# Kernel tuning notes

Hardware: AMD Instinct MI355X
Metric: run time of the kernel (lower is better)

The kernel has to match this reference:

```python
import jax, jax.numpy as jnp
import numpy as np

DM = 1024      # dmodel
HQK = 1024     # heads*dq == heads*dk == heads*dv
FF = 4096
VOCAB = 32000
NCAT = 75
DK = 64        # per-head dk used for 1/sqrt(dk) scaling
UNK_IDX = 1
EPS = 1e-5


def pos_encoding(n, dm):
    pos = jnp.arange(n, dtype=jnp.float32)[:, None]                  # [n,1]
    power = jnp.arange(0, dm, 2, dtype=jnp.float32) / dm             # [dm/2]
    denom = jnp.power(10000.0, power)                                # [dm/2]
    ang = pos / denom                                                # [n,dm/2]
    # even cols = sin, odd cols = cos (interleaved)
    return jnp.stack([jnp.sin(ang), jnp.cos(ang)], axis=-1).reshape(n, dm)


def layernorm(x, g, b):
    mu = jnp.mean(x, axis=-1, keepdims=True)
    var = jnp.var(x, axis=-1, keepdims=True)
    return (x - mu) * jax.lax.rsqrt(var + EPS) * g + b


def setup_inputs() -> dict:
    key = jax.random.key(0)
    ks = jax.random.split(key, 16)
    s = 0.02
    inp = {
        "input_indices": jax.random.randint(ks[0], (8, 2048), 0, VOCAB),
        "emb": jax.random.normal(ks[1], (VOCAB, DM), jnp.float32) * s,
        "Wq": jax.random.normal(ks[2], (DM, HQK), jnp.float32) * s,
        "bq": jnp.zeros((HQK,), jnp.float32),
        "Wk": jax.random.normal(ks[3], (DM, HQK), jnp.float32) * s,
        "bk": jnp.zeros((HQK,), jnp.float32),
        "Wv": jax.random.normal(ks[4], (DM, HQK), jnp.float32) * s,
        "bv": jnp.zeros((HQK,), jnp.float32),
        "Wu": jax.random.normal(ks[5], (HQK, DM), jnp.float32) * s,
        "bu": jnp.zeros((DM,), jnp.float32),
        "g1": jnp.ones((DM,), jnp.float32),
        "be1": jnp.zeros((DM,), jnp.float32),
        "W1": jax.random.normal(ks[6], (DM, FF), jnp.float32) * s,
        "b1": jnp.zeros((FF,), jnp.float32),
        "W2": jax.random.normal(ks[7], (FF, DM), jnp.float32) * s,
        "b2": jnp.zeros((DM,), jnp.float32),
        "g2": jnp.ones((DM,), jnp.float32),
        "be2": jnp.zeros((DM,), jnp.float32),
        "W3": jax.random.normal(ks[8], (DM, DM // 2), jnp.float32) * s,
        "b3": jnp.zeros((DM // 2,), jnp.float32),
        "W4": jax.random.normal(ks[9], (DM // 2, NCAT), jnp.float32) * s,
        "b4": jnp.zeros((NCAT,), jnp.float32),
        "g3": jnp.ones((NCAT,), jnp.float32),
        "be3": jnp.zeros((NCAT,), jnp.float32),
    }
    return inp


def reference(input_indices, emb, Wq, bq, Wk, bk, Wv, bv, Wu, bu, g1, be1,
              W1, b1, W2, b2, g2, be2, W3, b3, W4, b4, g3, be3):
    d, n = input_indices.shape
    idx = jnp.where(input_indices >= VOCAB, UNK_IDX, input_indices)
    x = emb[idx] + pos_encoding(n, DM)[None]                          # [d,n,dm]
    # attention WITHOUT softmax: scores = QK^T/sqrt(dk); attn = scores @ V
    q = x @ Wq + bq
    k = x @ Wk + bk
    v = x @ Wv + bv
    scores = jnp.einsum('bnd,bmd->bnm', q, k) / (DK ** 0.5)           # [d,n,n]
    attn = jnp.einsum('bnm,bmd->bnd', scores, v)                      # [d,n,hdv]
    u = attn @ Wu + bu
    h1 = layernorm(x + u, g1, be1)
    ffo = jax.nn.relu(h1 @ W1 + b1) @ W2 + b2
    h2 = layernorm(h1 + ffo, g2, be2)
    logits = jax.nn.relu(h2 @ W3 + b3) @ W4 + b4                      # [d,n,75]
    return jax.nn.sigmoid(layernorm(logits, g3, be3))
```

## Files before the change

kernel.cpp:

```cpp
#include <hip/hip_runtime.h>
#include <hip/hip_fp16.h>
#include <math.h>

#define DM    1024
#define FFD   4096
#define VOCAB 32000
#define NCAT  75
#define UNK_IDX 1
#define EPS   1e-5f
#define NB    8
#define SEQ   2048
#define T_TOK (NB*SEQ)

using u16   = unsigned short;
using half_t = _Float16;
using half8 = __attribute__((ext_vector_type(8))) _Float16;
using f32x4 = __attribute__((ext_vector_type(4))) float;

struct alignas(8) h4 { half_t s[4]; };

__device__ __forceinline__ void async16(const half_t* g, half_t* l) {
    __builtin_amdgcn_global_load_lds(
        (const __attribute__((address_space(1))) void*)g,
        (__attribute__((address_space(3))) void*)l,
        16, 0, 0);
}

__global__ __launch_bounds__(256)
void embed_pos_kernel(const int* __restrict__ idx,
                      const float* __restrict__ emb,
                      float* __restrict__ xf, half_t* __restrict__ xh)
{
    int gid = blockIdx.x * blockDim.x + threadIdx.x;
    if (gid >= T_TOK * DM) return;
    int dcol = gid & (DM - 1);
    int tok  = gid >> 10;
    int t    = tok & (SEQ - 1);
    int id = idx[tok];
    if (id >= VOCAB || id < 0) id = UNK_IDX;
    int p = dcol >> 1;
    float power = (float)p / 512.0f;
    float denom = powf(10000.0f, power);
    float ang = (float)t / denom;
    float pe = (dcol & 1) ? cosf(ang) : sinf(ang);
    float v = emb[(long long)id * DM + dcol] + pe;
    xf[gid] = v;
    xh[gid] = (half_t)v;
}

__global__ __launch_bounds__(256)
void transpose_h_kernel(const float* __restrict__ in, half_t* __restrict__ out,
                        int K, int N, int Npad)
{
    __shared__ float t[32][33];
    int n0 = blockIdx.x * 32, k0 = blockIdx.y * 32;
    int tx = threadIdx.x & 31, ty = threadIdx.x >> 5;
#pragma unroll
    for (int i = 0; i < 4; i++) {
        int k = k0 + ty + i * 8, n = n0 + tx;
        t[ty + i * 8][tx] = (k < K && n < N) ? in[(long long)k * N + n] : 0.f;
    }
    __syncthreads();
#pragma unroll
    for (int i = 0; i < 4; i++) {
        int n = n0 + ty + i * 8, k = k0 + tx;
        if (n < Npad && k < K)
            out[(long long)n * K + k] = (half_t)t[tx][ty + i * 8];
    }
}

__global__ __launch_bounds__(128)
void pad_bias_kernel(const float* __restrict__ b, float* __restrict__ bp)
{
    int i = threadIdx.x;
    bp[i] = (i < NCAT) ? b[i] : 0.f;
}

template<int OUT_MODE>
__global__ __launch_bounds__(256)
void gemm_nt(const half_t* __restrict__ A, const half_t* __restrict__ B,
             const float* __restrict__ bias, void* __restrict__ Cout,
             int M, int N, int K, int ld,
             long long sA, long long sB, long long sC,
             float scale, int do_relu)
{
    A += (long long)blockIdx.z * sA;
    B += (long long)blockIdx.z * sB;
    const int tid  = threadIdx.x;
    const int lane = tid & 63;
    const int w    = tid >> 6;
    const int wm   = w >> 1, wn = w & 1;
    const long long row0 = (long long)blockIdx.y * 128;
    const long long col0 = (long long)blockIdx.x * 128;

    __shared__ half_t smem[4 * 4096];
    half_t* const As = smem;
    half_t* const Bs = smem + 2 * 4096;

    f32x4 acc[4][4];
    const f32x4 zero = {0.f, 0.f, 0.f, 0.f};
#pragma unroll
    for (int i = 0; i < 4; i++)
#pragma unroll
        for (int j = 0; j < 4; j++) acc[i][j] = zero;

    const int ldrow = lane >> 2;
    const int swcol = (((lane & 3) << 3)) ^ ((ldrow & 3) << 3);
    const int fr    = lane & 15;
    const int kk8   = (lane >> 4) << 3;

    const int KT = K / 32;

#define ISSUE(k0, buf)                                                         \
    {                                                                          \
        _Pragma("unroll")                                                      \
        for (int it = 0; it < 2; ++it) {                                       \
            int rb = (it * 4 + w) * 16;                                        \
            long long ao = (row0 + rb + ldrow) * (long long)ld + (k0) + swcol; \
            long long bo = (col0 + rb + ldrow) * (long long)ld + (k0) + swcol; \
            async16(A + ao, As + (buf) * 4096 + rb * 32);                      \
            async16(B + bo, Bs + (buf) * 4096 + rb * 32);                      \
        }                                                                      \
    }

    ISSUE(0, 0);
    for (int kt = 0; kt < KT; ++kt) {
        const int cur = kt & 1;
        __syncthreads();
        if (kt + 1 < KT) ISSUE((kt + 1) * 32, cur ^ 1);

        half8 af[4], bf[4];
#pragma unroll
        for (int i = 0; i < 4; ++i) {
            int r   = wm * 64 + i * 16 + fr;
            int off = cur * 4096 + r * 32 + (kk8 ^ ((r & 3) << 3));
            af[i] = *(const half8*)(As + off);
        }
#pragma unroll
        for (int j = 0; j < 4; ++j) {
            int r   = wn * 64 + j * 16 + fr;
            int off = cur * 4096 + r * 32 + (kk8 ^ ((r & 3) << 3));
            bf[j] = *(const half8*)(Bs + off);
        }
#pragma unroll
        for (int i = 0; i < 4; ++i)
#pragma unroll
            for (int j = 0; j < 4; ++j)
                acc[i][j] = __builtin_amdgcn_mfma_f32_16x16x32_f16(
                    af[i], bf[j], acc[i][j], 0, 0, 0);
    }
#undef ISSUE

    const int qr = (lane >> 4) * 4;
    const int lc = lane & 15;
#pragma unroll
    for (int i = 0; i < 4; ++i) {
#pragma unroll
        for (int j = 0; j < 4; ++j) {
            long long gc = col0 + wn * 64 + j * 16 + lc;
            float bv = bias ? bias[gc] : 0.f;
            if (OUT_MODE == 2) {
                long long gr = row0 + wm * 64 + i * 16 + qr;
                int b  = (int)(gr >> 11);
                int tl = (int)(gr & (SEQ - 1));
                h4 pk;
#pragma unroll
                for (int r = 0; r < 4; ++r) {
                    float f = acc[i][j][r] * scale + bv;
                    if (do_relu) f = fmaxf(f, 0.f);
                    pk.s[r] = (half_t)f;
                }
                half_t* C = (half_t*)Cout;
                *(h4*)(C + (long long)b * N * SEQ + gc * SEQ + tl) = pk;
            } else if (OUT_MODE == 1) {
                half_t* C = (half_t*)Cout + blockIdx.z * sC;
#pragma unroll
                for (int r = 0; r < 4; ++r) {
                    long long gr = row0 + wm * 64 + i * 16 + qr + r;
                    float f = acc[i][j][r] * scale + bv;
                    if (do_relu) f = fmaxf(f, 0.f);
                    C[gr * N + gc] = (half_t)f;
                }
            } else {
                float* C = (float*)Cout + blockIdx.z * sC;
#pragma unroll
                for (int r = 0; r < 4; ++r) {
                    long long gr = row0 + wm * 64 + i * 16 + qr + r;
                    float f = acc[i][j][r] * scale + bv;
                    if (do_relu) f = fmaxf(f, 0.f);
                    C[gr * N + gc] = f;
                }
            }
        }
    }
}

__global__ __launch_bounds__(256)
void reduce2_bias_kernel(const float* __restrict__ s0, const float* __restrict__ s1,
                         const float* __restrict__ bias, float* __restrict__ out,
                         int n4)
{
    int i = blockIdx.x * blockDim.x + threadIdx.x;
    if (i >= n4) return;
    float4 a = ((const float4*)s0)[i];
    float4 b = ((const float4*)s1)[i];
    int c4 = (i * 4) & (DM - 1);
    float4 bb = *(const float4*)(bias + c4);
    float4 r;
    r.x = a.x + b.x + bb.x;
    r.y = a.y + b.y + bb.y;
    r.z = a.z + b.z + bb.z;
    r.w = a.w + b.w + bb.w;
    ((float4*)out)[i] = r;
}

__global__ __launch_bounds__(256)
void add_ln_kernel(const float* __restrict__ X, const float* __restrict__ Y,
                   const float* __restrict__ g, const float* __restrict__ b,
                   float* __restrict__ outf, half_t* __restrict__ outh)
{
    int row = blockIdx.x;
    int tid = threadIdx.x;
    const float* xr = X + (long long)row * DM;
    const float* yr = Y + (long long)row * DM;
    float v[4];
    float s = 0.f, s2 = 0.f;
#pragma unroll
    for (int i = 0; i < 4; i++) {
        int c = tid + i * 256;
        v[i] = xr[c] + yr[c];
        s  += v[i];
        s2 += v[i] * v[i];
    }
#pragma unroll
    for (int o = 1; o < 64; o <<= 1) {
        s  += __shfl_xor(s,  o, 64);
        s2 += __shfl_xor(s2, o, 64);
    }
    __shared__ float rs[4], rs2[4], stats[2];
    int wid = tid >> 6;
    if ((tid & 63) == 0) { rs[wid] = s; rs2[wid] = s2; }
    __syncthreads();
    if (tid == 0) {
        float S  = rs[0] + rs[1] + rs[2] + rs[3];
        float S2 = rs2[0] + rs2[1] + rs2[2] + rs2[3];
        float mean = S / (float)DM;
        float var  = S2 / (float)DM - mean * mean;
        stats[0] = mean;
        stats[1] = rsqrtf(var + EPS);
    }
    __syncthreads();
    float mean = stats[0], rstd = stats[1];
#pragma unroll
    for (int i = 0; i < 4; i++) {
        int c = tid + i * 256;
        float o = (v[i] - mean) * rstd * g[c] + b[c];
        if (outf) outf[(long long)row * DM + c] = o;
        outh[(long long)row * DM + c] = (half_t)o;
    }
}

__global__ __launch_bounds__(64)
void ln75_sigmoid_kernel(const float* __restrict__ L,
                         const float* __restrict__ g, const float* __restrict__ b,
                         float* __restrict__ out)
{
    int row = blockIdx.x;
    int t   = threadIdx.x;
    const float* lr = L + (long long)row * 128;
    float e0 = (t < NCAT) ? lr[t] : 0.f;
    float e1 = (t + 64 < NCAT) ? lr[t + 64] : 0.f;
    float s  = e0 + e1;
    float s2 = e0 * e0 + e1 * e1;
#pragma unroll
    for (int o = 1; o < 64; o <<= 1) {
        s  += __shfl_xor(s,  o, 64);
        s2 += __shfl_xor(s2, o, 64);
    }
    float mean = s / (float)NCAT;
    float var  = s2 / (float)NCAT - mean * mean;
    float rstd = rsqrtf(var + EPS);
    if (t < NCAT) {
        float z = (e0 - mean) * rstd * g[t] + b[t];
        out[(long long)row * NCAT + t] = 1.f / (1.f + expf(-z));
    }
    if (t + 64 < NCAT) {
        float z = (e1 - mean) * rstd * g[t + 64] + b[t + 64];
        out[(long long)row * NCAT + t + 64] = 1.f / (1.f + expf(-z));
    }
}

extern "C" void kernel_launch(void* const* d_in, const int* in_sizes, int n_in,
                              void* d_out, int out_size, void* d_ws, size_t ws_size,
                              hipStream_t stream)
{
    const int*   idx = (const int*)  d_in[0];
    const float* emb = (const float*)d_in[1];
    const float* Wq  = (const float*)d_in[2];
    const float* bq  = (const float*)d_in[3];
    const float* Wk  = (const float*)d_in[4];
    const float* bk  = (const float*)d_in[5];
    const float* Wv  = (const float*)d_in[6];
    const float* bv  = (const float*)d_in[7];
    const float* Wu  = (const float*)d_in[8];
    const float* bu  = (const float*)d_in[9];
    const float* g1  = (const float*)d_in[10];
    const float* be1 = (const float*)d_in[11];
    const float* W1  = (const float*)d_in[12];
    const float* b1  = (const float*)d_in[13];
    const float* W2  = (const float*)d_in[14];
    const float* b2  = (const float*)d_in[15];
    const float* g2  = (const float*)d_in[16];
    const float* be2 = (const float*)d_in[17];
    const float* W3  = (const float*)d_in[18];
    const float* b3  = (const float*)d_in[19];
    const float* W4  = (const float*)d_in[20];
    const float* b4  = (const float*)d_in[21];
    const float* g3  = (const float*)d_in[22];
    const float* be3 = (const float*)d_in[23];

    const long long TD  = (long long)T_TOK * DM;
    char* p = (char*)d_ws;
    char* R_A = p; p += TD * 4;
    char* R_B = p; p += TD * 2;
    char* R_C = p; p += TD * 2;
    char* R_D = p; p += TD * 4;
    char* R_E = p; p += TD * 4;
    char* R_F = p; p += (long long)NB * DM * DM * 4;
    char* R_G = p; p += (long long)T_TOK * 128 * 4;
    half_t* Wqh = (half_t*)p; p += DM*DM*2;
    half_t* Wkh = (half_t*)p; p += DM*DM*2;
    half_t* Wvh = (half_t*)p; p += DM*DM*2;
    half_t* Wuh = (half_t*)p; p += DM*DM*2;
    half_t* W1h = (half_t*)p; p += (long long)FFD*DM*2;
    half_t* W2h = (half_t*)p; p += (long long)DM*FFD*2;
    half_t* W3h = (half_t*)p; p += 512*DM*2;
    half_t* W4h = (half_t*)p; p += 128*512*2;
    float*  b4p = (float*)p;  p += 128*4;

    float*  Xf   = (float*)R_A;
    float*  ffo  = (float*)R_A;
    half_t* Xh   = (half_t*)R_B;
    half_t* attn = (half_t*)R_B;
    half_t* h2h  = (half_t*)R_B;
    half_t* Qh   = (half_t*)R_C;
    half_t* h1h  = (half_t*)R_C;
    half_t* Kt   = (half_t*)R_D;
    float*  u    = (float*)R_D;
    half_t* f1h  = (half_t*)R_D;
    half_t* Vt   = (half_t*)R_E;
    float*  h1f  = (float*)R_E;
    half_t* ktv  = (half_t*)R_F;
    float*  slc  = (float*)R_F;
    half_t* l1h  = (half_t*)R_F;
    float*  LOG  = (float*)R_G;
    float*  out  = (float*)d_out;

    dim3 blk(256);

    transpose_h_kernel<<<dim3(32, 32),  blk, 0, stream>>>(Wq, Wqh, DM, DM, DM);
    transpose_h_kernel<<<dim3(32, 32),  blk, 0, stream>>>(Wk, Wkh, DM, DM, DM);
    transpose_h_kernel<<<dim3(32, 32),  blk, 0, stream>>>(Wv, Wvh, DM, DM, DM);
    transpose_h_kernel<<<dim3(32, 32),  blk, 0, stream>>>(Wu, Wuh, DM, DM, DM);
    transpose_h_kernel<<<dim3(128, 32), blk, 0, stream>>>(W1, W1h, DM, FFD, FFD);
    transpose_h_kernel<<<dim3(32, 128), blk, 0, stream>>>(W2, W2h, FFD, DM, DM);
    transpose_h_kernel<<<dim3(16, 32),  blk, 0, stream>>>(W3, W3h, DM, 512, 512);
    transpose_h_kernel<<<dim3(4, 16),   blk, 0, stream>>>(W4, W4h, 512, NCAT, 128);
    pad_bias_kernel<<<1, 128, 0, stream>>>(b4, b4p);

    embed_pos_kernel<<<(T_TOK * DM + 255) / 256, blk, 0, stream>>>(idx, emb, Xf, Xh);

    gemm_nt<1><<<dim3(8, 128, 1), blk, 0, stream>>>(Xh, Wqh, bq, Qh,
        T_TOK, DM, DM, DM, 0, 0, 0, 1.f, 0);
    gemm_nt<2><<<dim3(8, 128, 1), blk, 0, stream>>>(Xh, Wkh, bk, Kt,
        T_TOK, DM, DM, DM, 0, 0, 0, 1.f, 0);
    gemm_nt<2><<<dim3(8, 128, 1), blk, 0, stream>>>(Xh, Wvh, bv, Vt,
        T_TOK, DM, DM, DM, 0, 0, 0, 1.f, 0);

    gemm_nt<1><<<dim3(8, 8, NB), blk, 0, stream>>>(Vt, Kt, nullptr, ktv,
        DM, DM, SEQ, SEQ, (long long)DM * SEQ, (long long)DM * SEQ, (long long)DM * DM, 0.125f, 0);

    gemm_nt<1><<<dim3(8, 16, NB), blk, 0, stream>>>(Qh, ktv, nullptr, attn,
        SEQ, DM, DM, DM, (long long)SEQ * DM, (long long)DM * DM, (long long)SEQ * DM, 1.f, 0);

    gemm_nt<0><<<dim3(8, 128, 1), blk, 0, stream>>>(attn, Wuh, bu, u,
        T_TOK, DM, DM, DM, 0, 0, 0, 1.f, 0);

    add_ln_kernel<<<T_TOK, blk, 0, stream>>>(Xf, u, g1, be1, h1f, h1h);

    for (int c = 0; c < 4; c++) {
        const half_t* h1c  = h1h + (long long)c * 4096 * DM;
        float*        ffoc = ffo + (long long)c * 4096 * DM;
        gemm_nt<1><<<dim3(32, 32, 1), blk, 0, stream>>>(h1c, W1h, b1, f1h,
            4096, FFD, DM, DM, 0, 0, 0, 1.f, 1);
        gemm_nt<0><<<dim3(8, 32, 2), blk, 0, stream>>>(f1h, W2h, nullptr, slc,
            4096, DM, 2048, FFD, 2048, 2048, (long long)4096 * DM, 1.f, 0);
        reduce2_bias_kernel<<<(4096 * DM / 4 + 255) / 256, blk, 0, stream>>>(
            slc, slc + (long long)4096 * DM, b2, ffoc, 4096 * DM / 4);
    }

    add_ln_kernel<<<T_TOK, blk, 0, stream>>>(h1f, ffo, g2, be2, nullptr, h2h);

    gemm_nt<1><<<dim3(4, 128, 1), blk, 0, stream>>>(h2h, W3h, b3, l1h,
        T_TOK, 512, DM, DM, 0, 0, 0, 1.f, 1);
    gemm_nt<0><<<dim3(1, 128, 1), blk, 0, stream>>>(l1h, W4h, b4p, LOG,
        T_TOK, 128, 512, 512, 0, 0, 0, 1.f, 0);

    ln75_sigmoid_kernel<<<T_TOK, 64, 0, stream>>>(LOG, g3, be3, out);
}
```

Baseline: 1.253 ms.

## Fold Wu into per-batch K^T V matrix, fuse residual, drop split-K FFN

Precomputes the positional encoding table once and vectorizes embedding and layernorm with float4 accesses. Reassociates the attention output projection, computing (K^T V)·Wu per batch so the per-token Wu GEMM disappears, and adds the residual inside the GEMM epilogue. The FFN now runs in two larger chunks without split-K, which removes the reduce kernel. Extra per-batch DMxDM GEMMs are added, and the fp16 rounding of the folded matrix may change numerics slightly.

Measured after the change: 1.212 ms. 1.03x faster.

```diff
diff --git a/kernel.cpp b/kernel.cpp
--- a/kernel.cpp
+++ b/kernel.cpp
@@ -27,25 +27,38 @@
 }
 
 __global__ __launch_bounds__(256)
-void embed_pos_kernel(const int* __restrict__ idx,
-                      const float* __restrict__ emb,
-                      float* __restrict__ xf, half_t* __restrict__ xh)
+void pe_kernel(float* __restrict__ pe)
 {
     int gid = blockIdx.x * blockDim.x + threadIdx.x;
-    if (gid >= T_TOK * DM) return;
+    if (gid >= SEQ * DM) return;
     int dcol = gid & (DM - 1);
-    int tok  = gid >> 10;
-    int t    = tok & (SEQ - 1);
-    int id = idx[tok];
-    if (id >= VOCAB || id < 0) id = UNK_IDX;
+    int t    = gid >> 10;
     int p = dcol >> 1;
     float power = (float)p / 512.0f;
     float denom = powf(10000.0f, power);
     float ang = (float)t / denom;
-    float pe = (dcol & 1) ? cosf(ang) : sinf(ang);
-    float v = emb[(long long)id * DM + dcol] + pe;
-    xf[gid] = v;
-    xh[gid] = (half_t)v;
+    pe[gid] = (dcol & 1) ? cosf(ang) : sinf(ang);
+}
+
+__global__ __launch_bounds__(256)
+void embed_pos_kernel(const int* __restrict__ idx,
+                      const float* __restrict__ emb,
+                      const float* __restrict__ pe,
+                      float* __restrict__ xf, half_t* __restrict__ xh)
+{
+    int gid4 = blockIdx.x * blockDim.x + threadIdx.x;
+    if (gid4 >= T_TOK * DM / 4) return;
+    int tok = gid4 >> 8;
+    int c4  = (gid4 & 255) << 2;
+    int t   = tok & (SEQ - 1);
+    int id = idx[tok];
+    if (id >= VOCAB || id < 0) id = UNK_IDX;
+    float4 e = *(const float4*)(emb + (long long)id * DM + c4);
+    float4 q = *(const float4*)(pe + (long long)t * DM + c4);
+    float4 v = make_float4(e.x + q.x, e.y + q.y, e.z + q.z, e.w + q.w);
+    *(float4*)(xf + (long long)tok * DM + c4) = v;
+    h4 pk = {{(half_t)v.x, (half_t)v.y, (half_t)v.z, (half_t)v.w}};
+    *(h4*)(xh + (long long)tok * DM + c4) = pk;
 }
 
 __global__ __launch_bounds__(256)
@@ -79,7 +92,8 @@
 template<int OUT_MODE>
 __global__ __launch_bounds__(256)
 void gemm_nt(const half_t* __restrict__ A, const half_t* __restrict__ B,
-             const float* __restrict__ bias, void* __restrict__ Cout,
+             const float* __restrict__ bias, const float* __restrict__ resid,
+             void* __restrict__ Cout,
              int M, int N, int K, int ld,
              long long sA, long long sB, long long sC,
              float scale, int do_relu)
@@ -153,6 +167,7 @@
 
     const int qr = (lane >> 4) * 4;
     const int lc = lane & 15;
+    const float* rz = resid ? resid + (long long)blockIdx.z * sC : nullptr;
 #pragma unroll
     for (int i = 0; i < 4; ++i) {
 #pragma unroll
@@ -188,6 +203,7 @@
                     long long gr = row0 + wm * 64 + i * 16 + qr + r;
                     float f = acc[i][j][r] * scale + bv;
                     if (do_relu) f = fmaxf(f, 0.f);
+                    if (rz) f += rz[gr * N + gc];
                     C[gr * N + gc] = f;
                 }
             }
@@ -196,42 +212,19 @@
 }
 
 __global__ __launch_bounds__(256)
-void reduce2_bias_kernel(const float* __restrict__ s0, const float* __restrict__ s1,
-                         const float* __restrict__ bias, float* __restrict__ out,
-                         int n4)
-{
-    int i = blockIdx.x * blockDim.x + threadIdx.x;
-    if (i >= n4) return;
-    float4 a = ((const float4*)s0)[i];
-    float4 b = ((const float4*)s1)[i];
-    int c4 = (i * 4) & (DM - 1);
-    float4 bb = *(const float4*)(bias + c4);
-    float4 r;
-    r.x = a.x + b.x + bb.x;
-    r.y = a.y + b.y + bb.y;
-    r.z = a.z + b.z + bb.z;
-    r.w = a.w + b.w + bb.w;
-    ((float4*)out)[i] = r;
-}
-
-__global__ __launch_bounds__(256)
 void add_ln_kernel(const float* __restrict__ X, const float* __restrict__ Y,
                    const float* __restrict__ g, const float* __restrict__ b,
                    float* __restrict__ outf, half_t* __restrict__ outh)
 {
     int row = blockIdx.x;
     int tid = threadIdx.x;
-    const float* xr = X + (long long)row * DM;
-    const float* yr = Y + (long long)row * DM;
-    float v[4];
-    float s = 0.f, s2 = 0.f;
-#pragma unroll
-    for (int i = 0; i < 4; i++) {
-        int c = tid + i * 256;
-        v[i] = xr[c] + yr[c];
-        s  += v[i];
-        s2 += v[i] * v[i];
-    }
+    float4 v = ((const float4*)(X + (long long)row * DM))[tid];
+    if (Y) {
+        float4 y = ((const float4*)(Y + (long long)row * DM))[tid];
+        v.x += y.x; v.y += y.y; v.z += y.z; v.w += y.w;
+    }
+    float s  = v.x + v.y + v.z + v.w;
+    float s2 = v.x * v.x + v.y * v.y + v.z * v.z + v.w * v.w;
 #pragma unroll
     for (int o = 1; o < 64; o <<= 1) {
         s  += __shfl_xor(s,  o, 64);
@@ -251,13 +244,16 @@
     }
     __syncthreads();
     float mean = stats[0], rstd = stats[1];
-#pragma unroll
-    for (int i = 0; i < 4; i++) {
-        int c = tid + i * 256;
-        float o = (v[i] - mean) * rstd * g[c] + b[c];
-        if (outf) outf[(long long)row * DM + c] = o;
-        outh[(long long)row * DM + c] = (half_t)o;
-    }
+    float4 gg = ((const float4*)g)[tid];
+    float4 bb = ((const float4*)b)[tid];
+    float4 o;
+    o.x = (v.x - mean) * rstd * gg.x + bb.x;
+    o.y = (v.y - mean) * rstd * gg.y + bb.y;
+    o.z = (v.z - mean) * rstd * gg.z + bb.z;
+    o.w = (v.w - mean) * rstd * gg.w + bb.w;
+    if (outf) ((float4*)(outf + (long long)row * DM))[tid] = o;
+    h4 pk = {{(half_t)o.x, (half_t)o.y, (half_t)o.z, (half_t)o.w}};
+    *(h4*)(outh + (long long)row * DM + tid * 4) = pk;
 }
 
 __global__ __launch_bounds__(64)
@@ -324,10 +320,12 @@
     char* R_A = p; p += TD * 4;
     char* R_B = p; p += TD * 2;
     char* R_C = p; p += TD * 2;
-    char* R_D = p; p += TD * 4;
+    char* R_D = p; p += TD * 2;
+    char* R_D2 = p; p += TD * 2;
     char* R_E = p; p += TD * 4;
     char* R_F = p; p += (long long)NB * DM * DM * 4;
     char* R_G = p; p += (long long)T_TOK * 128 * 4;
+    float* pe = (float*)p; p += (long long)SEQ * DM * 4;
     half_t* Wqh = (half_t*)p; p += DM*DM*2;
     half_t* Wkh = (half_t*)p; p += DM*DM*2;
     half_t* Wvh = (half_t*)p; p += DM*DM*2;
@@ -341,17 +339,16 @@
     float*  Xf   = (float*)R_A;
     float*  ffo  = (float*)R_A;
     half_t* Xh   = (half_t*)R_B;
-    half_t* attn = (half_t*)R_B;
     half_t* h2h  = (half_t*)R_B;
     half_t* Qh   = (half_t*)R_C;
     half_t* h1h  = (half_t*)R_C;
     half_t* Kt   = (half_t*)R_D;
-    float*  u    = (float*)R_D;
+    half_t* Vt   = (half_t*)R_D2;
     half_t* f1h  = (half_t*)R_D;
-    half_t* Vt   = (half_t*)R_E;
+    float*  usum = (float*)R_E;
     float*  h1f  = (float*)R_E;
-    half_t* ktv  = (half_t*)R_F;
-    float*  slc  = (float*)R_F;
+    half_t* ktv2 = (half_t*)R_F;
+    half_t* M2t  = (half_t*)(R_F + (long long)NB*DM*DM*2);
     half_t* l1h  = (half_t*)R_F;
     float*  LOG  = (float*)R_G;
     float*  out  = (float*)d_out;
@@ -367,43 +364,42 @@
     transpose_h_kernel<<<dim3(16, 32),  blk, 0, stream>>>(W3, W3h, DM, 512, 512);
     transpose_h_kernel<<<dim3(4, 16),   blk, 0, stream>>>(W4, W4h, 512, NCAT, 128);
     pad_bias_kernel<<<1, 128, 0, stream>>>(b4, b4p);
-
-    embed_pos_kernel<<<(T_TOK * DM + 255) / 256, blk, 0, stream>>>(idx, emb, Xf, Xh);
-
-    gemm_nt<1><<<dim3(8, 128, 1), blk, 0, stream>>>(Xh, Wqh, bq, Qh,
+    pe_kernel<<<(SEQ * DM + 255) / 256, blk, 0, stream>>>(pe);
+
+    embed_pos_kernel<<<(T_TOK * DM / 4 + 255) / 256, blk, 0, stream>>>(idx, emb, pe, Xf, Xh);
+
+    gemm_nt<1><<<dim3(8, 128, 1), blk, 0, stream>>>(Xh, Wqh, bq, nullptr, Qh,
         T_TOK, DM, DM, DM, 0, 0, 0, 1.f, 0);
-    gemm_nt<2><<<dim3(8, 128, 1), blk, 0, stream>>>(Xh, Wkh, bk, Kt,
+    gemm_nt<2><<<dim3(8, 128, 1), blk, 0, stream>>>(Xh, Wkh, bk, nullptr, Kt,
         T_TOK, DM, DM, DM, 0, 0, 0, 1.f, 0);
-    gemm_nt<2><<<dim3(8, 128, 1), blk, 0, stream>>>(Xh, Wvh, bv, Vt,
+    gemm_nt<2><<<dim3(8, 128, 1), blk, 0, stream>>>(Xh, Wvh, bv, nullptr, Vt,
         T_TOK, DM, DM, DM, 0, 0, 0, 1.f, 0);
 
-    gemm_nt<1><<<dim3(8, 8, NB), blk, 0, stream>>>(Vt, Kt, nullptr, ktv,
+    gemm_nt<1><<<dim3(8, 8, NB), blk, 0, stream>>>(Kt, Vt, nullptr, nullptr, ktv2,
         DM, DM, SEQ, SEQ, (long long)DM * SEQ, (long long)DM * SEQ, (long long)DM * DM, 0.125f, 0);
 
-    gemm_nt<1><<<dim3(8, 16, NB), blk, 0, stream>>>(Qh, ktv, nullptr, attn,
+    gemm_nt<1><<<dim3(8, 8, NB), blk, 0, stream>>>(Wuh, ktv2, nullptr, nullptr, M2t,
+        DM, DM, DM, DM, 0, (long long)DM * DM, (long long)DM * DM, 1.f, 0);
+
+    gemm_nt<0><<<dim3(8, 16, NB), blk, 0, stream>>>(Qh, M2t, bu, Xf, usum,
         SEQ, DM, DM, DM, (long long)SEQ * DM, (long long)DM * DM, (long long)SEQ * DM, 1.f, 0);
 
-    gemm_nt<0><<<dim3(8, 128, 1), blk, 0, stream>>>(attn, Wuh, bu, u,
-        T_TOK, DM, DM, DM, 0, 0, 0, 1.f, 0);
-
-    add_ln_kernel<<<T_TOK, blk, 0, stream>>>(Xf, u, g1, be1, h1f, h1h);
-
-    for (int c = 0; c < 4; c++) {
-        const half_t* h1c  = h1h + (long long)c * 4096 * DM;
-        float*        ffoc = ffo + (long long)c * 4096 * DM;
-        gemm_nt<1><<<dim3(32, 32, 1), blk, 0, stream>>>(h1c, W1h, b1, f1h,
-            4096, FFD, DM, DM, 0, 0, 0, 1.f, 1);
-        gemm_nt<0><<<dim3(8, 32, 2), blk, 0, stream>>>(f1h, W2h, nullptr, slc,
-            4096, DM, 2048, FFD, 2048, 2048, (long long)4096 * DM, 1.f, 0);
-        reduce2_bias_kernel<<<(4096 * DM / 4 + 255) / 256, blk, 0, stream>>>(
-            slc, slc + (long long)4096 * DM, b2, ffoc, 4096 * DM / 4);
+    add_ln_kernel<<<T_TOK, blk, 0, stream>>>(usum, nullptr, g1, be1, h1f, h1h);
+
+    for (int c = 0; c < 2; c++) {
+        const half_t* h1c  = h1h + (long long)c * 8192 * DM;
+        float*        ffoc = ffo + (long long)c * 8192 * DM;
+        gemm_nt<1><<<dim3(32, 64, 1), blk, 0, stream>>>(h1c, W1h, b1, nullptr, f1h,
+            8192, FFD, DM, DM, 0, 0, 0, 1.f, 1);
+        gemm_nt<0><<<dim3(8, 64, 1), blk, 0, stream>>>(f1h, W2h, b2, nullptr, ffoc,
+            8192, DM, FFD, FFD, 0, 0, 0, 1.f, 0);
     }
 
     add_ln_kernel<<<T_TOK, blk, 0, stream>>>(h1f, ffo, g2, be2, nullptr, h2h);
 
-    gemm_nt<1><<<dim3(4, 128, 1), blk, 0, stream>>>(h2h, W3h, b3, l1h,
+    gemm_nt<1><<<dim3(4, 128, 1), blk, 0, stream>>>(h2h, W3h, b3, nullptr, l1h,
         T_TOK, 512, DM, DM, 0, 0, 0, 1.f, 1);
-    gemm_nt<0><<<dim3(1, 128, 1), blk, 0, stream>>>(l1h, W4h, b4p, LOG,
+    gemm_nt<0><<<dim3(1, 128, 1), blk, 0, stream>>>(l1h, W4h, b4p, nullptr, LOG,
         T_TOK, 128, 512, 512, 0, 0, 0, 1.f, 0);
 
     ln75_sigmoid_kernel<<<T_TOK, 64, 0, stream>>>(LOG, g3, be3, out);
```
